# Optimization experiments

Hardware: AMD Instinct MI355X
Metric: run time of the kernel (lower is better)

## Reference

```python
import math
import jax, jax.numpy as jnp
from jax import lax
import numpy as np

SQRT2 = 1.4142135623730951
LR_MLP = 0.01


def _blur_kernel():
    k = jnp.array([1., 3., 3., 1.], dtype=jnp.float32)
    k = k[:, None] * k[None, :]
    return k / jnp.sum(k)


def upfirdn2d(x, kernel, up, pad0, pad1):
    # x: (B,C,H,W). Matches torch upfirdn2d_native (flip kernel, zero-upsample, pad, correlate).
    B, C, H, W = x.shape
    x = x.reshape(B * C, 1, H, W)
    k = jnp.flip(kernel, (0, 1))[None, None]
    p1 = pad1 + (up - 1)  # lax lhs_dilation omits trailing zeros of upfirdn upsampling
    out = lax.conv_general_dilated(x, k, (1, 1), ((pad0, p1), (pad0, p1)), lhs_dilation=(up, up))
    return out.reshape(B, C, out.shape[-2], out.shape[-1])


def pixel_norm(x, eps=1e-6):
    norm = jnp.sqrt(jnp.sum(x * x, axis=1, keepdims=True))
    norm = norm / math.sqrt(x.shape[1])
    return x / (norm + eps)


def fused_act(x, b):
    return jax.nn.leaky_relu(x + b[None, :, None, None], 0.2) * SQRT2


def mod_conv(x, w, sw, sb, lat, demodulate, up):
    # w: (Cout,Cin,kh,kw); sw: (Cin, style_ch) equalized-lr linear; lat: (B, style_ch)
    Cout, Cin, kh, kw = w.shape
    s = lat @ (sw.T * (1.0 / math.sqrt(sw.shape[1]))) + sb  # (B, Cin), bias_init=1
    wm = (w * (1.0 / math.sqrt(Cin * kh * kw)))[None] * s[:, None, :, None, None]
    if demodulate:
        d = lax.rsqrt(jnp.sum(wm * wm, axis=(2, 3, 4)) + 1e-8)
        wm = wm * d[:, :, None, None, None]
    if up:
        # per-sample conv_transpose(stride=2, pad=0) == dilated conv with flipped kernel
        def f(xi, wi):
            return lax.conv_general_dilated(xi[None], jnp.flip(wi, (2, 3)), (1, 1),
                                            ((kh - 1, kh - 1), (kw - 1, kw - 1)),
                                            lhs_dilation=(2, 2))[0]
        out = jax.vmap(f)(x, wm)
        out = upfirdn2d(out, _blur_kernel() * 4.0, 1, 1, 1)  # Blur pad=(1,1), k*factor^2
    else:
        pad = kh // 2
        def f(xi, wi):
            return lax.conv_general_dilated(xi[None], wi, (1, 1), ((pad, pad), (pad, pad)))[0]
        out = jax.vmap(f)(x, wm)
    return out


def style_mapping(z, W, Bv):
    x = pixel_norm(z)
    sc = 1.0 / math.sqrt(W.shape[-1])
    for i in range(W.shape[0]):
        x = jax.nn.leaky_relu(x @ (W[i].T * sc) + Bv[i] * LR_MLP, 0.2) * SQRT2
    return x


def setup_inputs() -> dict:
    key = jax.random.key(0)
    ks = jax.random.split(key, 32)
    B = 32
    inp = {
        'z': jax.random.normal(ks[0], (B, 512), jnp.float32),
        'mlp_w': jax.random.normal(ks[1], (8, 512, 512), jnp.float32),
        'mlp_b': jax.random.normal(ks[2], (8, 512), jnp.float32),
        'const_input': jax.random.normal(ks[3], (1, 512, 4, 4), jnp.float32),
        'conv_w': jax.random.normal(ks[4], (9, 512, 512, 3, 3), jnp.float32),
        'conv_style_w': jax.random.normal(ks[5], (9, 512, 512), jnp.float32),
        'conv_style_b': jnp.ones((9, 512), jnp.float32),
        'noise_w': jax.random.normal(ks[6], (9,), jnp.float32),
        'act_bias': jnp.zeros((9, 512), jnp.float32),
        'torgb_w': jax.random.normal(ks[7], (5, 3, 512, 1, 1), jnp.float32),
        'torgb_style_w': jax.random.normal(ks[8], (5, 512, 512), jnp.float32),
        'torgb_style_b': jnp.ones((5, 512), jnp.float32),
        'torgb_bias': jnp.zeros((5, 3), jnp.float32),
    }
    sizes = [4, 8, 8, 16, 16, 32, 32, 64, 64]
    for i, s in enumerate(sizes):
        inp[f'noise{i}'] = jax.random.normal(ks[10 + i], (B, 1, s, s), jnp.float32)
    return inp


def reference(z, mlp_w, mlp_b, const_input, conv_w, conv_style_w, conv_style_b,
              noise_w, act_bias, torgb_w, torgb_style_w, torgb_style_b, torgb_bias,
              noise0, noise1, noise2, noise3, noise4, noise5, noise6, noise7, noise8):
    noises = [noise0, noise1, noise2, noise3, noise4, noise5, noise6, noise7, noise8]
    w = style_mapping(z, mlp_w, mlp_b)  # single style injection -> same w for all layers
    B = z.shape[0]
    x = jnp.tile(const_input, (B, 1, 1, 1))

    def sconv(x, i, up):
        out = mod_conv(x, conv_w[i], conv_style_w[i], conv_style_b[i], w, True, up)
        out = out + noise_w[i] * noises[i]
        return fused_act(out, act_bias[i])

    def trgb(x, j):
        out = mod_conv(x, torgb_w[j], torgb_style_w[j], torgb_style_b[j], w, False, False)
        return out + torgb_bias[j][None, :, None, None]

    x = sconv(x, 0, False)
    skip = trgb(x, 0)
    bk = _blur_kernel() * 4.0
    for r in range(4):  # resolutions 8,16,32,64
        x = sconv(x, 1 + 2 * r, True)
        x = sconv(x, 2 + 2 * r, False)
        skip = trgb(x, r + 1) + upfirdn2d(skip, bk, 2, 2, 1)  # UpsampleUpFIRDn pad=(2,1)
    return skip  # (B,3,64,64)
```

## Files before the change

kernel.cpp:

```cpp
#include <hip/hip_runtime.h>
#include <hip/hip_bf16.h>
#include <cstdio>
#include <math.h>


static constexpr int NB = 32;
static constexpr float SQRT2F      = 1.41421356237309515f;
static constexpr float INV_SQRT512 = 0.04419417382415922f;
static constexpr float INV_SQRT4608= 0.014731391274719742f;

typedef __hip_bfloat16 bf16;
typedef __attribute__((ext_vector_type(8))) short bf16x8;
typedef __attribute__((ext_vector_type(4))) float f32x4;

__device__ __forceinline__ float lrelu_s2(float v){ return (v > 0.f ? v : 0.2f*v) * SQRT2F; }
__device__ __forceinline__ float bf_lo(unsigned u){ unsigned v = u << 16; return __builtin_bit_cast(float, v); }
__device__ __forceinline__ float bf_hi(unsigned u){ unsigned v = u & 0xffff0000u; return __builtin_bit_cast(float, v); }
__device__ __forceinline__ unsigned packbf2(float a, float b){
  bf16 ha = __float2bfloat16(a), hb = __float2bfloat16(b);
  unsigned short ra = __builtin_bit_cast(unsigned short, ha);
  unsigned short rb = __builtin_bit_cast(unsigned short, hb);
  return (unsigned)ra | ((unsigned)rb << 16);
}

__global__ void k_mapping(const float* __restrict__ z, const float* __restrict__ mlp_w,
                          const float* __restrict__ mlp_b, float* __restrict__ wlat){
  __shared__ float xb[512], yb[512], red[256];
  int b = blockIdx.x, t = threadIdx.x;
  float z0 = z[b*512 + t], z1 = z[b*512 + t + 256];
  red[t] = z0*z0 + z1*z1;
  __syncthreads();
  for(int s = 128; s > 0; s >>= 1){ if(t < s) red[t] += red[t+s]; __syncthreads(); }
  float norm = sqrtf(red[0]) * INV_SQRT512;
  float inv = 1.f / (norm + 1e-6f);
  xb[t] = z0*inv; xb[t+256] = z1*inv;
  __syncthreads();
  for(int l = 0; l < 8; l++){
    const float* Wl = mlp_w + (size_t)l*512*512;
    const float* bl = mlp_b + l*512;
    for(int oo = 0; oo < 2; oo++){
      int o = t + oo*256;
      const float4* wr = (const float4*)(Wl + (size_t)o*512);
      float acc = 0.f;
      #pragma unroll 4
      for(int k = 0; k < 128; k++){
        float4 w4 = wr[k];
        acc += w4.x*xb[4*k] + w4.y*xb[4*k+1] + w4.z*xb[4*k+2] + w4.w*xb[4*k+3];
      }
      yb[o] = lrelu_s2(acc*INV_SQRT512 + bl[o]*0.01f);
    }
    __syncthreads();
    xb[t] = yb[t]; xb[t+256] = yb[t+256];
    __syncthreads();
  }
  wlat[b*512+t] = xb[t]; wlat[b*512+t+256] = xb[t+256];
}

__global__ void k_styles(const float* __restrict__ wlat,
                         const float* __restrict__ csw, const float* __restrict__ csb,
                         const float* __restrict__ tsw, const float* __restrict__ tsb,
                         float* __restrict__ s_conv, float* __restrict__ s_trgb){
  int gid = blockIdx.x*256 + threadIdx.x;
  int l = gid >> 14;
  int b = (gid >> 9) & 31;
  int i = gid & 511;
  const float* row; float bias, wsc;
  if(l < 9){ row = csw + ((size_t)l*512 + i)*512; bias = csb[l*512+i]; wsc = INV_SQRT4608; }
  else     { int lt = l-9; row = tsw + ((size_t)lt*512 + i)*512; bias = tsb[lt*512+i]; wsc = INV_SQRT512; }
  const float4* r4 = (const float4*)row;
  const float4* w4 = (const float4*)(wlat + b*512);
  float acc = 0.f;
  #pragma unroll 4
  for(int k = 0; k < 128; k++){
    float4 a = w4[k], c = r4[k];
    acc += a.x*c.x + a.y*c.y + a.z*c.z + a.w*c.w;
  }
  float s = (acc*INV_SQRT512 + bias) * wsc;
  if(l < 9) s_conv[((size_t)l*32 + b)*512 + i] = s;
  else      s_trgb[((size_t)(l-9)*32 + b)*512 + i] = s;
}

__global__ void k_prep(const float* __restrict__ cw, float* __restrict__ wsq,
                       bf16* __restrict__ wB){
  int gid = blockIdx.x*256 + threadIdx.x;
  const float* p = cw + (size_t)gid*9;
  int l = gid >> 18;
  int oi = gid & 0x3ffff;
  float v[9]; float a = 0.f;
  #pragma unroll
  for(int t = 0; t < 9; t++){ v[t] = p[t]; a += v[t]*v[t]; }
  wsq[gid] = a;
  #pragma unroll
  for(int tap = 0; tap < 9; tap++)
    wB[((size_t)(l*9 + tap) << 18) + oi] = __float2bfloat16(v[tap]);
}

__global__ void k_demod(const float* __restrict__ s_conv, const float* __restrict__ wsq,
                        float* __restrict__ d_conv){
  __shared__ float s2[512];
  int l = blockIdx.x/32, b = blockIdx.x%32, t = threadIdx.x;
  size_t base = ((size_t)l*32 + b)*512;
  float v0 = s_conv[base + t], v1 = s_conv[base + t + 256];
  s2[t] = v0*v0; s2[t+256] = v1*v1;
  __syncthreads();
  for(int oo = 0; oo < 2; oo++){
    int o = t + oo*256;
    const float4* wr = (const float4*)(wsq + ((size_t)l*512 + o)*512);
    float acc = 0.f;
    #pragma unroll 4
    for(int k = 0; k < 128; k++){
      float4 w = wr[k];
      acc += w.x*s2[4*k] + w.y*s2[4*k+1] + w.z*s2[4*k+2] + w.w*s2[4*k+3];
    }
    d_conv[base + o] = rsqrtf(acc + 1e-8f);
  }
}

__global__ void k_ratio(const float* __restrict__ s_conv, const float* __restrict__ s_trgb,
                        float* __restrict__ rat){
  int gid = blockIdx.x*256 + threadIdx.x;
  int lt = gid >> 14;
  if(lt >= 4){ rat[gid] = 1.0f; return; }
  int b = (gid >> 9) & 31;
  int i = gid & 511;
  int cl = 1 + 2*lt;
  float st = s_trgb[((size_t)lt*32 + b)*512 + i];
  float sc = s_conv[((size_t)cl*32 + b)*512 + i];
  rat[gid] = (sc != 0.f) ? st/sc : 0.f;
}

__global__ void k_init(const float* __restrict__ ci, const float* __restrict__ s_conv,
                       bf16* __restrict__ act){
  int gid = blockIdx.x*256 + threadIdx.x;
  int c = gid & 511; int px = (gid >> 9) & 15; int b = gid >> 13;
  act[gid] = __float2bfloat16(ci[c*16 + px] * s_conv[b*512 + c]);
}

template<bool UP>
__global__ __launch_bounds__(256, 2)
void k_conv(const bf16* __restrict__ act, const bf16* __restrict__ wL,
            const float* __restrict__ dL, const float* __restrict__ noise,
            const float* __restrict__ nw_ptr, const float* __restrict__ ab,
            const float* __restrict__ sN, bf16* __restrict__ outp,
            int Hin, int Mblocks){
  const int q8 = gridDim.x >> 3;
  const int swz = (blockIdx.x & 7)*q8 + (blockIdx.x >> 3);
  const int nb = swz & 3, mb = swz >> 2;
  if(mb >= Mblocks) return;
  const int mbase = mb*128, nbase = nb*128;

  int py = 0, px = 0;
  int OHy, OHx;
  if(UP){
    int cls = blockIdx.z; py = cls >> 1; px = cls & 1;
    OHy = Hin + 1 - py; OHx = Hin + 1 - px;
  } else {
    OHy = Hin; OHx = Hin;
  }
  const int pixN = OHy*OHx;
  const int Mtot = NB*pixN;
  if(mbase >= Mtot) return;

  __shared__ short As[128*64];
  __shared__ short Bs[128*64];
  const int t = threadIdx.x;
  const int row  = t >> 1;
  const int half = t & 1;
  const int r7   = row & 7;

  int m = mbase + row;
  const bool mval = (m < Mtot);
  int mm = mval ? m : 0;
  const int gb = mm / pixN; int rem = mm % pixN;
  const int gY = rem / OHx, gX = rem % OHx;

  const int wid = t >> 6;
  const int mrow0 = (wid >> 1)*64;
  const int ncol0 = (wid & 1)*64;
  const int lr = t & 15;
  const int ks = (t & 63) >> 4;
  const int lr7 = lr & 7;
  const int sw0 = (ks ^ lr7)*8;
  const int sw1 = ((4 + ks) ^ lr7)*8;

  int wsl[4];
  #pragma unroll
  for(int j = 0; j < 4; j++) wsl[j] = ((half*4 + j) ^ r7)*8;

  f32x4 acc[4][4];
  #pragma unroll
  for(int i = 0; i < 4; i++)
    #pragma unroll
    for(int j = 0; j < 4; j++) acc[i][j] = (f32x4){0.f,0.f,0.f,0.f};

  int dyl[3], dxl[3], ndy, ndx;
  if(UP){
    if(py == 0){ dyl[0]=0; dyl[1]=2; ndy=2; } else { dyl[0]=1; ndy=1; }
    if(px == 0){ dxl[0]=0; dxl[1]=2; ndx=2; } else { dxl[0]=1; ndx=1; }
  } else {
    dyl[0]=0; dyl[1]=1; dyl[2]=2; ndy=3;
    dxl[0]=0; dxl[1]=1; dxl[2]=2; ndx=3;
  }
  const int TT = ndy*ndx;

  const bf16* browB = wL + ((size_t)(nbase + row) << 9) + half*32;

  for(int tt = 0; tt < TT; tt++){
    const int dy = dyl[tt/ndx], dx = dxl[tt%ndx];
    const int tap = dy*3 + dx;
    bool aok = false; const bf16* aptr = act;
    {
      int yy, xx;
      if(UP){ yy = gY - ((dy - py) >> 1); xx = gX - ((dx - px) >> 1); }
      else  { yy = gY + dy - 1;           xx = gX + dx - 1; }
      if(mval && (unsigned)yy < (unsigned)Hin && (unsigned)xx < (unsigned)Hin){
        aok = true;
        aptr = act + ((size_t)((gb*Hin + yy)*Hin + xx) << 9) + half*32;
      }
    }
    const bf16* bptr = browB + ((size_t)tap << 18);

    uint4 pa[4], pb[4];
    #pragma unroll
    for(int j = 0; j < 4; j++){
      pa[j] = aok ? *(const uint4*)(aptr + j*8) : make_uint4(0u,0u,0u,0u);
      pb[j] = *(const uint4*)(bptr + j*8);
    }

    #pragma unroll
    for(int c = 0; c < 8; c++){
      asm volatile("" ::: "memory");
      __builtin_amdgcn_s_barrier();
      #pragma unroll
      for(int j = 0; j < 4; j++){
        *(uint4*)&As[row*64 + wsl[j]] = pa[j];
        *(uint4*)&Bs[row*64 + wsl[j]] = pb[j];
      }
      uint4 na[4], nb4[4];
      if(c < 7){
        const int koff = (c+1)*64;
        #pragma unroll
        for(int j = 0; j < 4; j++){
          na[j]  = aok ? *(const uint4*)(aptr + koff + j*8) : make_uint4(0u,0u,0u,0u);
          nb4[j] = *(const uint4*)(bptr + koff + j*8);
        }
      }
      asm volatile("s_waitcnt lgkmcnt(0)" ::: "memory");
      __builtin_amdgcn_s_barrier();
      #pragma unroll
      for(int h = 0; h < 2; h++){
        const int swr = h ? sw1 : sw0;
        bf16x8 af[4], bfr[4];
        #pragma unroll
        for(int f = 0; f < 4; f++){
          af[f]  = *(const bf16x8*)&As[(mrow0 + f*16 + lr)*64 + swr];
          bfr[f] = *(const bf16x8*)&Bs[(ncol0 + f*16 + lr)*64 + swr];
        }
        #pragma unroll
        for(int mf = 0; mf < 4; mf++)
          #pragma unroll
          for(int nf = 0; nf < 4; nf++)
            acc[mf][nf] = __builtin_amdgcn_mfma_f32_16x16x32_bf16(af[mf], bfr[nf], acc[mf][nf], 0, 0, 0);
      }
      if(c < 7){
        #pragma unroll
        for(int j = 0; j < 4; j++){ pa[j] = na[j]; pb[j] = nb4[j]; }
      }
    }
  }

  const float nwv = UP ? 0.f : *nw_ptr;
  const int U = 2*Hin + 1;
  #pragma unroll
  for(int mf = 0; mf < 4; mf++){
    #pragma unroll
    for(int r = 0; r < 4; r++){
      int me = mbase + mrow0 + mf*16 + ks*4 + r;
      if(me >= Mtot) continue;
      int b = me / pixN; int rem2 = me % pixN; int y = rem2 / OHx, x = rem2 % OHx;
      const float* drow = dL + b*512;
      bf16* orow;
      float nz = 0.f; const float* srow = nullptr;
      if(UP){
        orow = outp + (((size_t)((b*U + 2*y + py))*U + (2*x + px)) << 9);
      } else {
        nz = nwv * noise[(b*OHy + y)*OHx + x];
        srow = sN + b*512;
        orow = outp + ((size_t)me << 9);
      }
      #pragma unroll
      for(int nf = 0; nf < 4; nf++){
        int n = nbase + ncol0 + nf*16 + lr;
        float val = acc[mf][nf][r] * drow[n];
        if(!UP) val = lrelu_s2(val + nz + ab[n]) * srow[n];
        orow[n] = __float2bfloat16(val);
      }
    }
  }
}

__global__ void k_blur(const bf16* __restrict__ u, const float* __restrict__ noise,
                       const float* __restrict__ nw_ptr, const float* __restrict__ ab,
                       const float* __restrict__ sN, bf16* __restrict__ act, int O){
  const int U = O + 1;
  size_t gid = (size_t)blockIdx.x*256 + threadIdx.x;
  size_t total = (size_t)NB*O*O*128;
  if(gid >= total) return;
  int c4 = gid & 127;
  size_t pix = gid >> 7;
  int X = pix % O; int Y = (pix/O) % O; int b = pix/((size_t)O*O);
  const float k1[4] = {1.f, 3.f, 3.f, 1.f};
  float4 a = make_float4(0.f,0.f,0.f,0.f);
  #pragma unroll
  for(int ky = 0; ky < 4; ky++){
    int yy = Y + ky - 1; if(yy < 0 || yy >= U) continue;
    #pragma unroll
    for(int kx = 0; kx < 4; kx++){
      int xx = X + kx - 1; if(xx < 0 || xx >= U) continue;
      float w = k1[ky]*k1[kx]*(1.f/16.f);
      uint2 u2 = *(const uint2*)(u + (((size_t)(b*U + yy)*U + xx) << 9) + c4*4);
      a.x += w*bf_lo(u2.x); a.y += w*bf_hi(u2.x);
      a.z += w*bf_lo(u2.y); a.w += w*bf_hi(u2.y);
    }
  }
  float nz = (*nw_ptr) * noise[(b*O + Y)*O + X];
  const float* abp4 = ab + c4*4;
  float4 s4 = *(const float4*)(sN + b*512 + c4*4);
  uint2 pk;
  pk.x = packbf2(lrelu_s2(a.x + nz + abp4[0])*s4.x, lrelu_s2(a.y + nz + abp4[1])*s4.y);
  pk.y = packbf2(lrelu_s2(a.z + nz + abp4[2])*s4.z, lrelu_s2(a.w + nz + abp4[3])*s4.w);
  *(uint2*)(act + (pix << 9) + c4*4) = pk;
}

__global__ void k_torgb(const bf16* __restrict__ act, const float* __restrict__ tw,
                        const float* __restrict__ ratL, const float* __restrict__ tbias,
                        float* __restrict__ dst, int H, int lt, int addflag){
  int wid = threadIdx.x >> 6, lane = threadIdx.x & 63;
  int pix = blockIdx.x*4 + wid;
  int npix = NB*H*H;
  if(pix >= npix) return;
  int b = pix/(H*H);
  const bf16* ap = act + ((size_t)pix << 9);
  const float* rp = ratL + (size_t)b*512;
  const float* w0 = tw + ((size_t)lt*3 + 0)*512;
  const float* w1 = tw + ((size_t)lt*3 + 1)*512;
  const float* w2 = tw + ((size_t)lt*3 + 2)*512;
  float a0 = 0.f, a1 = 0.f, a2 = 0.f;
  #pragma unroll
  for(int j = 0; j < 8; j++){
    int i = lane + j*64;
    float xs = __bfloat162float(ap[i])*rp[i];
    a0 += xs*w0[i]; a1 += xs*w1[i]; a2 += xs*w2[i];
  }
  for(int off = 32; off > 0; off >>= 1){
    a0 += __shfl_xor(a0, off);
    a1 += __shfl_xor(a1, off);
    a2 += __shfl_xor(a2, off);
  }
  if(lane == 0){
    int rem = pix % (H*H);
    size_t o0 = ((size_t)(b*3 + 0)*H*H) + rem;
    size_t o1 = ((size_t)(b*3 + 1)*H*H) + rem;
    size_t o2 = ((size_t)(b*3 + 2)*H*H) + rem;
    float b0 = tbias[lt*3+0], b1 = tbias[lt*3+1], b2 = tbias[lt*3+2];
    if(addflag){ dst[o0] += a0 + b0; dst[o1] += a1 + b1; dst[o2] += a2 + b2; }
    else       { dst[o0]  = a0 + b0; dst[o1]  = a1 + b1; dst[o2]  = a2 + b2; }
  }
}

__global__ void k_skipup(const float* __restrict__ sin, float* __restrict__ sout, int h){
  const int O = 2*h;
  int gid = blockIdx.x*256 + threadIdx.x;
  int total = NB*3*O*O;
  if(gid >= total) return;
  int X = gid % O; int Y = (gid/O) % O; int c = (gid/(O*O)) % 3; int b = gid/(3*O*O);
  const float k1[4] = {1.f, 3.f, 3.f, 1.f};
  float acc = 0.f;
  for(int ky = (Y & 1); ky < 4; ky += 2){
    int ty = Y + ky - 2;
    if(ty < 0) continue;
    int y = ty >> 1; if(y >= h) continue;
    for(int kx = (X & 1); kx < 4; kx += 2){
      int tx = X + kx - 2;
      if(tx < 0) continue;
      int x = tx >> 1; if(x >= h) continue;
      acc += k1[ky]*k1[kx]*(1.f/16.f) * sin[((size_t)(b*3 + c)*h + y)*h + x];
    }
  }
  sout[gid] = acc;
}

extern "C" void kernel_launch(void* const* d_in, const int* in_sizes, int n_in,
                              void* d_out, int out_size, void* d_ws, size_t ws_size,
                              hipStream_t stream){
  const float* z     = (const float*)d_in[0];
  const float* mlp_w = (const float*)d_in[1];
  const float* mlp_b = (const float*)d_in[2];
  const float* cinp  = (const float*)d_in[3];
  const float* conv_w= (const float*)d_in[4];
  const float* csw   = (const float*)d_in[5];
  const float* csb   = (const float*)d_in[6];
  const float* nwp   = (const float*)d_in[7];
  const float* abp   = (const float*)d_in[8];
  const float* tw    = (const float*)d_in[9];
  const float* tsw   = (const float*)d_in[10];
  const float* tsb   = (const float*)d_in[11];
  const float* tb    = (const float*)d_in[12];
  const float* noise[9];
  for(int i = 0; i < 9; i++) noise[i] = (const float*)d_in[13 + i];

  const size_t UMAX = (size_t)32*65*65*512;
  char* base = (char*)d_ws;
  size_t off = 0;
  bf16* buf0 = (bf16*)(base + off); off += UMAX*2;
  bf16* buf1 = (bf16*)(base + off); off += UMAX*2;
  bf16* wB   = (bf16*)(base + off); off += (size_t)9*9*512*512*2;
  float* wsq = (float*)(base + off); off += (size_t)9*512*512*4;
  float* wlat= (float*)(base + off); off += (size_t)32*512*4;
  float* sconv=(float*)(base + off); off += (size_t)9*32*512*4;
  float* dconv=(float*)(base + off); off += (size_t)9*32*512*4;
  float* strgb=(float*)(base + off); off += (size_t)5*32*512*4;
  float* rat  =(float*)(base + off); off += (size_t)5*32*512*4;
  float* skipA=(float*)(base + off); off += (size_t)32*3*64*64*4;
  float* skipB=(float*)(base + off); off += (size_t)32*3*64*64*4;
  if(ws_size < off){
    fprintf(stderr, "kernel_launch: ws too small (%zu < %zu)\n", ws_size, off);
    return;
  }
  float* out = (float*)d_out;

  k_mapping<<<32, 256, 0, stream>>>(z, mlp_w, mlp_b, wlat);
  k_styles <<<896, 256, 0, stream>>>(wlat, csw, csb, tsw, tsb, sconv, strgb);
  k_prep   <<<9216, 256, 0, stream>>>(conv_w, wsq, wB);
  k_demod  <<<288, 256, 0, stream>>>(sconv, wsq, dconv);
  k_ratio  <<<320, 256, 0, stream>>>(sconv, strgb, rat);
  k_init   <<<1024, 256, 0, stream>>>(cinp, sconv, buf0);

  auto conv_noup = [&](const bf16* in, bf16* o, int H, int layer, const float* sN){
    int M = 32*H*H; int Mb = (M + 127)/128;
    int Gx = ((Mb*4 + 7)/8)*8;
    k_conv<false><<<dim3(Gx,1,1), 256, 0, stream>>>(in, wB + ((size_t)layer*9 << 18),
        dconv + (size_t)layer*NB*512, noise[layer], nwp + layer, abp + layer*512, sN, o, H, Mb);
  };
  auto conv_up = [&](const bf16* in, bf16* o, int Hin, int layer){
    int Mmax = 32*(Hin+1)*(Hin+1); int Mb = (Mmax + 127)/128;
    int Gx = ((Mb*4 + 7)/8)*8;
    k_conv<true><<<dim3(Gx,1,4), 256, 0, stream>>>(in, wB + ((size_t)layer*9 << 18),
        dconv + (size_t)layer*NB*512, nullptr, nullptr, nullptr, nullptr, o, Hin, Mb);
  };
  auto blur = [&](const bf16* u, bf16* o, int O, int layer, const float* sN){
    size_t total = (size_t)32*O*O*128;
    k_blur<<<(unsigned)((total + 255)/256), 256, 0, stream>>>(u, noise[layer], nwp + layer,
        abp + layer*512, sN, o, O);
  };
  auto torgb = [&](const bf16* act, float* dst, int H, int lt, int add){
    int npix = 32*H*H;
    k_torgb<<<(npix + 3)/4, 256, 0, stream>>>(act, tw, rat + (size_t)lt*NB*512, tb, dst, H, lt, add);
  };
  auto skipup = [&](const float* sin, float* sout, int h){
    int total = 32*3*(2*h)*(2*h);
    k_skipup<<<(total + 255)/256, 256, 0, stream>>>(sin, sout, h);
  };

  const float* S = sconv;
  const float* sT4 = strgb + (size_t)4*NB*512;

  conv_noup(buf0, buf1, 4, 0, S + (size_t)1*NB*512);
  torgb(buf1, skipA, 4, 0, 0);

  conv_up(buf1, buf0, 4, 1);
  blur(buf0, buf1, 8, 1, S + (size_t)2*NB*512);
  conv_noup(buf1, buf0, 8, 2, S + (size_t)3*NB*512);
  skipup(skipA, skipB, 4);
  torgb(buf0, skipB, 8, 1, 1);

  conv_up(buf0, buf1, 8, 3);
  blur(buf1, buf0, 16, 3, S + (size_t)4*NB*512);
  conv_noup(buf0, buf1, 16, 4, S + (size_t)5*NB*512);
  skipup(skipB, skipA, 8);
  torgb(buf1, skipA, 16, 2, 1);

  conv_up(buf1, buf0, 16, 5);
  blur(buf0, buf1, 32, 5, S + (size_t)6*NB*512);
  conv_noup(buf1, buf0, 32, 6, S + (size_t)7*NB*512);
  skipup(skipA, skipB, 16);
  torgb(buf0, skipB, 32, 3, 1);

  conv_up(buf0, buf1, 32, 7);
  blur(buf1, buf0, 64, 7, S + (size_t)8*NB*512);
  conv_noup(buf0, buf1, 64, 8, sT4);
  skipup(skipB, out, 32);
  torgb(buf1, out, 64, 4, 1);
}
```

Before: 2.248 ms.

## Pipeline conv K-loop across taps, specialize up-conv classes, separable blur

Reorders conv weights to [layer][out][tap*512+in] so each output row's taps are contiguous. The conv main loop now prefetches two K-chunks ahead across tap boundaries with double-buffered registers, and the tap count becomes a compile-time constant. The four up-sampling parity classes become separate template instantiations launched individually, sized to their exact M instead of padding all to the largest class. The 4x4 blur is split into vertical and horizontal passes through a bf16 temp buffer, which adds an extra round-trip and extra bf16 rounding.

```diff
diff --git a/kernel.cpp b/kernel.cpp
--- a/kernel.cpp
+++ b/kernel.cpp
@@ -86,13 +86,15 @@
   const float* p = cw + (size_t)gid*9;
   int l = gid >> 18;
   int oi = gid & 0x3ffff;
+  int o = oi >> 9, i = oi & 511;
   float v[9]; float a = 0.f;
   #pragma unroll
   for(int t = 0; t < 9; t++){ v[t] = p[t]; a += v[t]*v[t]; }
   wsq[gid] = a;
+  size_t base = ((size_t)l*512 + o)*4608 + i;
   #pragma unroll
   for(int tap = 0; tap < 9; tap++)
-    wB[((size_t)(l*9 + tap) << 18) + oi] = __float2bfloat16(v[tap]);
+    wB[base + tap*512] = __float2bfloat16(v[tap]);
 }
 
 __global__ void k_demod(const float* __restrict__ s_conv, const float* __restrict__ wsq,
@@ -136,27 +138,48 @@
   act[gid] = __float2bfloat16(ci[c*16 + px] * s_conv[b*512 + c]);
 }
 
-template<bool UP>
+template<bool UP, int PY, int PX>
+__device__ __forceinline__ void tap_ptr(int tt, bool mval, int gY, int gX, int gb,
+                                        int Hin, const bf16* __restrict__ act, int half,
+                                        bool& ok, const bf16*& ap, int& tapidx){
+  int dy, dx;
+  if(UP){
+    constexpr int NDX = (PX==0) ? 2 : 1;
+    int iy = (NDX==2) ? (tt>>1) : tt;
+    int ix = tt & (NDX-1);
+    dy = (PY==0) ? iy*2 : 1;
+    dx = (PX==0) ? ix*2 : 1;
+  } else {
+    dy = (tt*11) >> 5; dx = tt - dy*3;
+  }
+  tapidx = dy*3 + dx;
+  int yy, xx;
+  if(UP){ yy = gY - ((dy - PY) >> 1); xx = gX - ((dx - PX) >> 1); }
+  else  { yy = gY + dy - 1;           xx = gX + dx - 1; }
+  ok = mval && ((unsigned)yy < (unsigned)Hin) && ((unsigned)xx < (unsigned)Hin);
+  ap = act + ((size_t)((gb*Hin + yy)*Hin + xx) << 9) + half*32;
+}
+
+template<bool UP, int PY, int PX>
 __global__ __launch_bounds__(256, 2)
 void k_conv(const bf16* __restrict__ act, const bf16* __restrict__ wL,
             const float* __restrict__ dL, const float* __restrict__ noise,
             const float* __restrict__ nw_ptr, const float* __restrict__ ab,
             const float* __restrict__ sN, bf16* __restrict__ outp,
             int Hin, int Mblocks){
+  constexpr int NDY = UP ? ((PY==0)?2:1) : 3;
+  constexpr int NDX = UP ? ((PX==0)?2:1) : 3;
+  constexpr int TT  = NDY*NDX;
+  constexpr int GTOT = TT*8;
+
   const int q8 = gridDim.x >> 3;
   const int swz = (blockIdx.x & 7)*q8 + (blockIdx.x >> 3);
   const int nb = swz & 3, mb = swz >> 2;
   if(mb >= Mblocks) return;
   const int mbase = mb*128, nbase = nb*128;
 
-  int py = 0, px = 0;
-  int OHy, OHx;
-  if(UP){
-    int cls = blockIdx.z; py = cls >> 1; px = cls & 1;
-    OHy = Hin + 1 - py; OHx = Hin + 1 - px;
-  } else {
-    OHy = Hin; OHx = Hin;
-  }
+  const int OHy = UP ? (Hin + 1 - PY) : Hin;
+  const int OHx = UP ? (Hin + 1 - PX) : Hin;
   const int pixN = OHy*OHx;
   const int Mtot = NB*pixN;
   if(mbase >= Mtot) return;
@@ -193,56 +216,48 @@
     #pragma unroll
     for(int j = 0; j < 4; j++) acc[i][j] = (f32x4){0.f,0.f,0.f,0.f};
 
-  int dyl[3], dxl[3], ndy, ndx;
-  if(UP){
-    if(py == 0){ dyl[0]=0; dyl[1]=2; ndy=2; } else { dyl[0]=1; ndy=1; }
-    if(px == 0){ dxl[0]=0; dxl[1]=2; ndx=2; } else { dxl[0]=1; ndx=1; }
-  } else {
-    dyl[0]=0; dyl[1]=1; dyl[2]=2; ndy=3;
-    dxl[0]=0; dxl[1]=1; dxl[2]=2; ndx=3;
-  }
-  const int TT = ndy*ndx;
-
-  const bf16* browB = wL + ((size_t)(nbase + row) << 9) + half*32;
-
-  for(int tt = 0; tt < TT; tt++){
-    const int dy = dyl[tt/ndx], dx = dxl[tt%ndx];
-    const int tap = dy*3 + dx;
-    bool aok = false; const bf16* aptr = act;
-    {
-      int yy, xx;
-      if(UP){ yy = gY - ((dy - py) >> 1); xx = gX - ((dx - px) >> 1); }
-      else  { yy = gY + dy - 1;           xx = gX + dx - 1; }
-      if(mval && (unsigned)yy < (unsigned)Hin && (unsigned)xx < (unsigned)Hin){
-        aok = true;
-        aptr = act + ((size_t)((gb*Hin + yy)*Hin + xx) << 9) + half*32;
-      }
-    }
-    const bf16* bptr = browB + ((size_t)tap << 18);
-
-    uint4 pa[4], pb[4];
-    #pragma unroll
-    for(int j = 0; j < 4; j++){
-      pa[j] = aok ? *(const uint4*)(aptr + j*8) : make_uint4(0u,0u,0u,0u);
-      pb[j] = *(const uint4*)(bptr + j*8);
-    }
-
+  const bf16* browB = wL + (size_t)(nbase + row)*4608 + half*32;
+
+  bool okC, okN; const bf16 *apC, *apN, *bpC, *bpN; int tapC, tapN;
+  tap_ptr<UP,PY,PX>(0, mval, gY, gX, gb, Hin, act, half, okC, apC, tapC);
+  bpC = browB + tapC*512;
+  if(TT > 1){
+    tap_ptr<UP,PY,PX>(1, mval, gY, gX, gb, Hin, act, half, okN, apN, tapN);
+    bpN = browB + tapN*512;
+  } else { okN = okC; apN = apC; bpN = bpC; }
+
+  uint4 pa[2][4], pb[2][4];
+  #pragma unroll
+  for(int j = 0; j < 4; j++){
+    pa[0][j] = okC ? *(const uint4*)(apC + j*8)      : make_uint4(0u,0u,0u,0u);
+    pb[0][j] = *(const uint4*)(bpC + j*8);
+    pa[1][j] = okC ? *(const uint4*)(apC + 64 + j*8) : make_uint4(0u,0u,0u,0u);
+    pb[1][j] = *(const uint4*)(bpC + 64 + j*8);
+  }
+
+  for(int tt = 0; tt < TT; ++tt){
     #pragma unroll
     for(int c = 0; c < 8; c++){
+      const int buf = c & 1;
       asm volatile("" ::: "memory");
       __builtin_amdgcn_s_barrier();
       #pragma unroll
       for(int j = 0; j < 4; j++){
-        *(uint4*)&As[row*64 + wsl[j]] = pa[j];
-        *(uint4*)&Bs[row*64 + wsl[j]] = pb[j];
+        *(uint4*)&As[row*64 + wsl[j]] = pa[buf][j];
+        *(uint4*)&Bs[row*64 + wsl[j]] = pb[buf][j];
       }
-      uint4 na[4], nb4[4];
-      if(c < 7){
-        const int koff = (c+1)*64;
-        #pragma unroll
-        for(int j = 0; j < 4; j++){
-          na[j]  = aok ? *(const uint4*)(aptr + koff + j*8) : make_uint4(0u,0u,0u,0u);
-          nb4[j] = *(const uint4*)(bptr + koff + j*8);
+      {
+        const int git = tt*8 + c + 2;
+        if(git < GTOT){
+          const bf16* ap = (c < 6) ? apC : apN;
+          const bf16* bp = (c < 6) ? bpC : bpN;
+          const bool  ok = (c < 6) ? okC : okN;
+          const int koff = ((c + 2) & 7)*64;
+          #pragma unroll
+          for(int j = 0; j < 4; j++){
+            pa[buf][j] = ok ? *(const uint4*)(ap + koff + j*8) : make_uint4(0u,0u,0u,0u);
+            pb[buf][j] = *(const uint4*)(bp + koff + j*8);
+          }
         }
       }
       asm volatile("s_waitcnt lgkmcnt(0)" ::: "memory");
@@ -262,10 +277,11 @@
           for(int nf = 0; nf < 4; nf++)
             acc[mf][nf] = __builtin_amdgcn_mfma_f32_16x16x32_bf16(af[mf], bfr[nf], acc[mf][nf], 0, 0, 0);
       }
-      if(c < 7){
-        #pragma unroll
-        for(int j = 0; j < 4; j++){ pa[j] = na[j]; pb[j] = nb4[j]; }
-      }
+    }
+    okC = okN; apC = apN; bpC = bpN;
+    if(tt + 2 < TT){
+      tap_ptr<UP,PY,PX>(tt+2, mval, gY, gX, gb, Hin, act, half, okN, apN, tapN);
+      bpN = browB + tapN*512;
     }
   }
 
@@ -282,7 +298,7 @@
       bf16* orow;
       float nz = 0.f; const float* srow = nullptr;
       if(UP){
-        orow = outp + (((size_t)((b*U + 2*y + py))*U + (2*x + px)) << 9);
+        orow = outp + (((size_t)((b*U + 2*y + PY))*U + (2*x + PX)) << 9);
       } else {
         nz = nwv * noise[(b*OHy + y)*OHx + x];
         srow = sN + b*512;
@@ -299,9 +315,32 @@
   }
 }
 
-__global__ void k_blur(const bf16* __restrict__ u, const float* __restrict__ noise,
-                       const float* __restrict__ nw_ptr, const float* __restrict__ ab,
-                       const float* __restrict__ sN, bf16* __restrict__ act, int O){
+__global__ void k_blurV(const bf16* __restrict__ u, bf16* __restrict__ tmp, int O){
+  const int U = O + 1;
+  size_t gid = (size_t)blockIdx.x*256 + threadIdx.x;
+  size_t total = (size_t)NB*O*U*128;
+  if(gid >= total) return;
+  int c4 = gid & 127;
+  size_t pix = gid >> 7;
+  int X = pix % U; int Y = (pix/U) % O; int b = pix/((size_t)O*U);
+  const float k1[4] = {0.25f, 0.75f, 0.75f, 0.25f};
+  float4 a = make_float4(0.f,0.f,0.f,0.f);
+  #pragma unroll
+  for(int ky = 0; ky < 4; ky++){
+    int yy = Y + ky - 1; if(yy < 0 || yy >= U) continue;
+    float w = k1[ky];
+    uint2 u2 = *(const uint2*)(u + (((size_t)(b*U + yy)*U + X) << 9) + c4*4);
+    a.x += w*bf_lo(u2.x); a.y += w*bf_hi(u2.x);
+    a.z += w*bf_lo(u2.y); a.w += w*bf_hi(u2.y);
+  }
+  uint2 pk;
+  pk.x = packbf2(a.x, a.y); pk.y = packbf2(a.z, a.w);
+  *(uint2*)(tmp + (pix << 9) + c4*4) = pk;
+}
+
+__global__ void k_blurH(const bf16* __restrict__ tmp, const float* __restrict__ noise,
+                        const float* __restrict__ nw_ptr, const float* __restrict__ ab,
+                        const float* __restrict__ sN, bf16* __restrict__ act, int O){
   const int U = O + 1;
   size_t gid = (size_t)blockIdx.x*256 + threadIdx.x;
   size_t total = (size_t)NB*O*O*128;
@@ -309,19 +348,15 @@
   int c4 = gid & 127;
   size_t pix = gid >> 7;
   int X = pix % O; int Y = (pix/O) % O; int b = pix/((size_t)O*O);
-  const float k1[4] = {1.f, 3.f, 3.f, 1.f};
+  const float k1[4] = {0.25f, 0.75f, 0.75f, 0.25f};
   float4 a = make_float4(0.f,0.f,0.f,0.f);
   #pragma unroll
-  for(int ky = 0; ky < 4; ky++){
-    int yy = Y + ky - 1; if(yy < 0 || yy >= U) continue;
-    #pragma unroll
-    for(int kx = 0; kx < 4; kx++){
-      int xx = X + kx - 1; if(xx < 0 || xx >= U) continue;
-      float w = k1[ky]*k1[kx]*(1.f/16.f);
-      uint2 u2 = *(const uint2*)(u + (((size_t)(b*U + yy)*U + xx) << 9) + c4*4);
-      a.x += w*bf_lo(u2.x); a.y += w*bf_hi(u2.x);
-      a.z += w*bf_lo(u2.y); a.w += w*bf_hi(u2.y);
-    }
+  for(int kx = 0; kx < 4; kx++){
+    int xx = X + kx - 1; if(xx < 0 || xx >= U) continue;
+    float w = k1[kx];
+    uint2 u2 = *(const uint2*)(tmp + (((size_t)(b*O + Y)*U + xx) << 9) + c4*4);
+    a.x += w*bf_lo(u2.x); a.y += w*bf_hi(u2.x);
+    a.z += w*bf_lo(u2.y); a.w += w*bf_hi(u2.y);
   }
   float nz = (*nw_ptr) * noise[(b*O + Y)*O + X];
   const float* abp4 = ab + c4*4;
@@ -414,7 +449,7 @@
   size_t off = 0;
   bf16* buf0 = (bf16*)(base + off); off += UMAX*2;
   bf16* buf1 = (bf16*)(base + off); off += UMAX*2;
-  bf16* wB   = (bf16*)(base + off); off += (size_t)9*9*512*512*2;
+  bf16* wB   = (bf16*)(base + off); off += (size_t)9*512*4608*2;
   float* wsq = (float*)(base + off); off += (size_t)9*512*512*4;
   float* wlat= (float*)(base + off); off += (size_t)32*512*4;
   float* sconv=(float*)(base + off); off += (size_t)9*32*512*4;
@@ -439,18 +474,24 @@
   auto conv_noup = [&](const bf16* in, bf16* o, int H, int layer, const float* sN){
     int M = 32*H*H; int Mb = (M + 127)/128;
     int Gx = ((Mb*4 + 7)/8)*8;
-    k_conv<false><<<dim3(Gx,1,1), 256, 0, stream>>>(in, wB + ((size_t)layer*9 << 18),
+    k_conv<false,0,0><<<dim3(Gx,1,1), 256, 0, stream>>>(in, wB + (size_t)layer*512*4608,
         dconv + (size_t)layer*NB*512, noise[layer], nwp + layer, abp + layer*512, sN, o, H, Mb);
   };
   auto conv_up = [&](const bf16* in, bf16* o, int Hin, int layer){
-    int Mmax = 32*(Hin+1)*(Hin+1); int Mb = (Mmax + 127)/128;
-    int Gx = ((Mb*4 + 7)/8)*8;
-    k_conv<true><<<dim3(Gx,1,4), 256, 0, stream>>>(in, wB + ((size_t)layer*9 << 18),
-        dconv + (size_t)layer*NB*512, nullptr, nullptr, nullptr, nullptr, o, Hin, Mb);
+    const bf16* w = wB + (size_t)layer*512*4608;
+    const float* d = dconv + (size_t)layer*NB*512;
+    auto gx = [&](int M){ int Mb = (M + 127)/128; return ((Mb*4 + 7)/8)*8; };
+    int Ma = 32*(Hin+1)*(Hin+1), Mb_ = 32*(Hin+1)*Hin, Mc = 32*Hin*(Hin+1), Md = 32*Hin*Hin;
+    k_conv<true,0,0><<<dim3(gx(Ma),1,1), 256, 0, stream>>>(in, w, d, nullptr, nullptr, nullptr, nullptr, o, Hin, (Ma+127)/128);
+    k_conv<true,0,1><<<dim3(gx(Mb_),1,1), 256, 0, stream>>>(in, w, d, nullptr, nullptr, nullptr, nullptr, o, Hin, (Mb_+127)/128);
+    k_conv<true,1,0><<<dim3(gx(Mc),1,1), 256, 0, stream>>>(in, w, d, nullptr, nullptr, nullptr, nullptr, o, Hin, (Mc+127)/128);
+    k_conv<true,1,1><<<dim3(gx(Md),1,1), 256, 0, stream>>>(in, w, d, nullptr, nullptr, nullptr, nullptr, o, Hin, (Md+127)/128);
   };
-  auto blur = [&](const bf16* u, bf16* o, int O, int layer, const float* sN){
-    size_t total = (size_t)32*O*O*128;
-    k_blur<<<(unsigned)((total + 255)/256), 256, 0, stream>>>(u, noise[layer], nwp + layer,
+  auto blur = [&](const bf16* u, bf16* tmp, bf16* o, int O, int layer, const float* sN){
+    size_t totV = (size_t)32*O*(O+1)*128;
+    size_t totH = (size_t)32*O*O*128;
+    k_blurV<<<(unsigned)((totV + 255)/256), 256, 0, stream>>>(u, tmp, O);
+    k_blurH<<<(unsigned)((totH + 255)/256), 256, 0, stream>>>(tmp, noise[layer], nwp + layer,
         abp + layer*512, sN, o, O);
   };
   auto torgb = [&](const bf16* act, float* dst, int H, int lt, int add){
@@ -469,25 +510,25 @@
   torgb(buf1, skipA, 4, 0, 0);
 
   conv_up(buf1, buf0, 4, 1);
-  blur(buf0, buf1, 8, 1, S + (size_t)2*NB*512);
-  conv_noup(buf1, buf0, 8, 2, S + (size_t)3*NB*512);
+  blur(buf0, buf1, buf0, 8, 1, S + (size_t)2*NB*512);
+  conv_noup(buf0, buf1, 8, 2, S + (size_t)3*NB*512);
   skipup(skipA, skipB, 4);
-  torgb(buf0, skipB, 8, 1, 1);
-
-  conv_up(buf0, buf1, 8, 3);
-  blur(buf1, buf0, 16, 3, S + (size_t)4*NB*512);
+  torgb(buf1, skipB, 8, 1, 1);
+
+  conv_up(buf1, buf0, 8, 3);
+  blur(buf0, buf1, buf0, 16, 3, S + (size_t)4*NB*512);
   conv_noup(buf0, buf1, 16, 4, S + (size_t)5*NB*512);
   skipup(skipB, skipA, 8);
   torgb(buf1, skipA, 16, 2, 1);
 
   conv_up(buf1, buf0, 16, 5);
-  blur(buf0, buf1, 32, 5, S + (size_t)6*NB*512);
-  conv_noup(buf1, buf0, 32, 6, S + (size_t)7*NB*512);
+  blur(buf0, buf1, buf0, 32, 5, S + (size_t)6*NB*512);
+  conv_noup(buf0, buf1, 32, 6, S + (size_t)7*NB*512);
   skipup(skipA, skipB, 16);
-  torgb(buf0, skipB, 32, 3, 1);
-
-  conv_up(buf0, buf1, 32, 7);
-  blur(buf1, buf0, 64, 7, S + (size_t)8*NB*512);
+  torgb(buf1, skipB, 32, 3, 1);
+
+  conv_up(buf1, buf0, 32, 7);
+  blur(buf0, buf1, buf0, 64, 7, S + (size_t)8*NB*512);
   conv_noup(buf0, buf1, 64, 8, sT4);
   skipup(skipB, out, 32);
   torgb(buf1, out, 64, 4, 1);
```

Result: slower. 5.122 ms (+127.8%).
